# Optimization experiments

Hardware: AMD Instinct MI355X
Metric: run time of the kernel (lower is better)

The kernel has to match this reference:

```python
import jax, jax.numpy as jnp
import numpy as np

D = 768  # hidden dim hard-coded in the module


def setup_inputs() -> dict:
    key = jax.random.key(0)
    k1, k2, k3, k4, k5 = jax.random.split(key, 5)
    N, M = 512, 512
    return {
        "text_output": jax.random.normal(k1, (N, D), dtype=jnp.float32),
        "visual_output": jax.random.normal(k2, (M, D), dtype=jnp.float32),
        "W1": jax.random.normal(k3, (D, D), dtype=jnp.float32),
        "W2": jax.random.normal(k4, (D, D), dtype=jnp.float32),
        "W3": jax.random.normal(k5, (D, D), dtype=jnp.float32),
    }


def reference(text_output, visual_output, W1, W2, W3):
    # C[n,m] = tanh( (text @ W1) . visual[m] )
    C = jnp.tanh((text_output @ W1) @ visual_output.T)            # (N, M)
    W2_text = text_output @ W2                                    # (N, D)
    W3_visual = visual_output @ W3.T                              # (M, D)
    # M[n,m,:] = tanh(W2_text[n] + W3_visual[m] * C[n,m])
    Mt = jnp.tanh(W2_text[:, None, :] + W3_visual[None, :, :] * C[..., None])  # (N, M, D)
    # score[n,m] = text[n] . M[n,m]  (replaces the per-row Python loop)
    score = jnp.einsum("nd,nmd->nm", text_output, Mt)             # (N, M)
    return score
```

## Files before the change

kernel.cpp:

```cpp
#include <hip/hip_runtime.h>

#define DD   768
#define NN   512
#define MM   512

#define PRE_K 2.88539008177792681472f

typedef _Float16 h8 __attribute__((ext_vector_type(8)));
typedef __attribute__((ext_vector_type(4))) float f32x4;

__device__ __forceinline__ float fexp(float x) { return __builtin_amdgcn_exp2f(x); }
__device__ __forceinline__ float frcp(float x) { return __builtin_amdgcn_rcpf(x); }
__device__ __forceinline__ float fast_tanh(float x) {
  return 1.0f - 2.0f * frcp(fexp(PRE_K * x) + 1.0f);
}

__device__ __forceinline__ void splitf(float x, ushort& h, ushort& l) {
  const _Float16 hh = (_Float16)x;
  const _Float16 ll = (_Float16)(x - (float)hh);
  h = __builtin_bit_cast(unsigned short, hh);
  l = __builtin_bit_cast(unsigned short, ll);
}

__global__ __launch_bounds__(256) void prep_kernel(
    const float* __restrict__ text, const float* __restrict__ visual,
    const float* __restrict__ W1, const float* __restrict__ W2,
    const float* __restrict__ W3,
    ushort* __restrict__ th, ushort* __restrict__ tl,
    ushort* __restrict__ vh, ushort* __restrict__ vl,
    ushort* __restrict__ w3h, ushort* __restrict__ w3l,
    ushort* __restrict__ w1th, ushort* __restrict__ w1tl,
    ushort* __restrict__ w2th, ushort* __restrict__ w2tl)
{
  __shared__ float Lt[32][33];
  const int b = blockIdx.x;
  const int t = threadIdx.x;

  if (b < 1344) {
    const float* src; ushort *dh, *dl; size_t off;
    if (b < 384)      { src = text;   dh = th;  dl = tl;  off = (size_t)b * 1024; }
    else if (b < 768) { src = visual; dh = vh;  dl = vl;  off = (size_t)(b - 384) * 1024; }
    else              { src = W3;     dh = w3h; dl = w3l; off = (size_t)(b - 768) * 1024; }
    const size_t i = off + (size_t)t * 4;
    const float4 v = *(const float4*)&src[i];
    ushort4 h, l;
    splitf(v.x, h.x, l.x); splitf(v.y, h.y, l.y);
    splitf(v.z, h.z, l.z); splitf(v.w, h.w, l.w);
    *(ushort4*)&dh[i] = h;
    *(ushort4*)&dl[i] = l;
  } else {
    const int tt = b - 1344;
    const bool second = tt >= 576;
    const int tile = second ? tt - 576 : tt;
    const float* W = second ? W2 : W1;
    ushort* oh = second ? w2th : w1th;
    ushort* ol = second ? w2tl : w1tl;
    const int k0 = (tile / 24) * 32, j0 = (tile % 24) * 32;
    {
      const int k = t >> 3, j4 = (t & 7) * 4;
      const float4 v = *(const float4*)&W[(size_t)(k0 + k) * DD + j0 + j4];
      Lt[j4 + 0][k] = v.x; Lt[j4 + 1][k] = v.y;
      Lt[j4 + 2][k] = v.z; Lt[j4 + 3][k] = v.w;
    }
    __syncthreads();
    {
      const int j = t >> 3, k4 = (t & 7) * 4;
      ushort4 h, l;
      splitf(Lt[j][k4 + 0], h.x, l.x); splitf(Lt[j][k4 + 1], h.y, l.y);
      splitf(Lt[j][k4 + 2], h.z, l.z); splitf(Lt[j][k4 + 3], h.w, l.w);
      *(ushort4*)&oh[(size_t)(j0 + j) * DD + k0 + k4] = h;
      *(ushort4*)&ol[(size_t)(j0 + j) * DD + k0 + k4] = l;
    }
  }
}

#define BK   32
#define LROW 40

__device__ __forceinline__ void gemm_core(
    const ushort* __restrict__ Ahg, const ushort* __restrict__ Alg,
    const ushort* __restrict__ Bhg, const ushort* __restrict__ Blg,
    int i0, int j0, int k0, int nsteps, f32x4* acc)
{
  __shared__ ushort As[2][2][64 * LROW];
  __shared__ ushort Bs[2][2][64 * LROW];

  const int tid  = threadIdx.x;
  const int row  = tid >> 2;
  const int ks8  = (tid & 3) * 8;
  const size_t ga = (size_t)(i0 + row) * DD + k0 + ks8;
  const size_t gb = (size_t)(j0 + row) * DD + k0 + ks8;
  const int ldsw = row * LROW + ks8;

  const int lane = tid & 63, wave = tid >> 6;
  const int r15 = lane & 15, quad = lane >> 4;
  const int fa = (wave * 16 + r15) * LROW + quad * 8;
  const int fb = r15 * LROW + quad * 8;

  h8 pah = *(const h8*)(Ahg + ga);
  h8 pal = *(const h8*)(Alg + ga);
  h8 pbh = *(const h8*)(Bhg + gb);
  h8 pbl = *(const h8*)(Blg + gb);

  int p = 0;
  *(h8*)&As[0][0][ldsw] = pah; *(h8*)&As[0][1][ldsw] = pal;
  *(h8*)&Bs[0][0][ldsw] = pbh; *(h8*)&Bs[0][1][ldsw] = pbl;
  __syncthreads();

  for (int s = 0; s < nsteps; ++s) {
    const bool more = (s + 1 < nsteps);
    if (more) {
      pah = *(const h8*)(Ahg + ga + (s + 1) * BK);
      pal = *(const h8*)(Alg + ga + (s + 1) * BK);
      pbh = *(const h8*)(Bhg + gb + (s + 1) * BK);
      pbl = *(const h8*)(Blg + gb + (s + 1) * BK);
    }
    const h8 a_h = *(const h8*)&As[p][0][fa];
    const h8 a_l = *(const h8*)&As[p][1][fa];
    h8 b_h[4], b_l[4];
    #pragma unroll
    for (int c = 0; c < 4; ++c) {
      b_h[c] = *(const h8*)&Bs[p][0][fb + c * 16 * LROW];
      b_l[c] = *(const h8*)&Bs[p][1][fb + c * 16 * LROW];
    }
    #pragma unroll
    for (int c = 0; c < 4; ++c)
      acc[c] = __builtin_amdgcn_mfma_f32_16x16x32_f16(a_h, b_h[c], acc[c], 0, 0, 0);
    #pragma unroll
    for (int c = 0; c < 4; ++c)
      acc[c] = __builtin_amdgcn_mfma_f32_16x16x32_f16(a_h, b_l[c], acc[c], 0, 0, 0);
    #pragma unroll
    for (int c = 0; c < 4; ++c)
      acc[c] = __builtin_amdgcn_mfma_f32_16x16x32_f16(a_l, b_h[c], acc[c], 0, 0, 0);
    if (more) {
      const int q = p ^ 1;
      *(h8*)&As[q][0][ldsw] = pah; *(h8*)&As[q][1][ldsw] = pal;
      *(h8*)&Bs[q][0][ldsw] = pbh; *(h8*)&Bs[q][1][ldsw] = pbl;
    }
    __syncthreads();
    p ^= 1;
  }
}

__global__ __launch_bounds__(256) void mfma1_kernel(
    const ushort* __restrict__ th, const ushort* __restrict__ tl,
    const ushort* __restrict__ vh, const ushort* __restrict__ vl,
    const ushort* __restrict__ w1th, const ushort* __restrict__ w1tl,
    const ushort* __restrict__ w2th, const ushort* __restrict__ w2tl,
    const ushort* __restrict__ w3h, const ushort* __restrict__ w3l,
    ushort* __restrict__ Ah, ushort* __restrict__ Al,
    float* __restrict__ kw2t, float* __restrict__ kw3v)
{
  const int z  = blockIdx.z;
  const int j0 = blockIdx.x * 64;
  const int i0 = blockIdx.y * 64;
  const ushort *Arh, *Arl, *Brh, *Brl;
  if (z == 0)      { Arh = th; Arl = tl; Brh = w1th; Brl = w1tl; }
  else if (z == 1) { Arh = th; Arl = tl; Brh = w2th; Brl = w2tl; }
  else             { Arh = vh; Arl = vl; Brh = w3h;  Brl = w3l;  }

  f32x4 acc[4];
  #pragma unroll
  for (int c = 0; c < 4; ++c) acc[c] = (f32x4){0.f, 0.f, 0.f, 0.f};
  gemm_core(Arh, Arl, Brh, Brl, i0, j0, 0, DD / BK, acc);

  const int lane = threadIdx.x & 63, wave = threadIdx.x >> 6;
  const int r15 = lane & 15, quad = lane >> 4;
  if (z == 0) {
    #pragma unroll
    for (int c = 0; c < 4; ++c)
      #pragma unroll
      for (int r = 0; r < 4; ++r) {
        const size_t o = (size_t)(i0 + wave * 16 + quad * 4 + r) * DD + j0 + c * 16 + r15;
        splitf(acc[c][r], Ah[o], Al[o]);
      }
  } else {
    float* Out = (z == 1) ? kw2t : kw3v;
    #pragma unroll
    for (int c = 0; c < 4; ++c)
      #pragma unroll
      for (int r = 0; r < 4; ++r)
        Out[(size_t)(i0 + wave * 16 + quad * 4 + r) * DD + j0 + c * 16 + r15] =
            acc[c][r] * PRE_K;
  }
}

__global__ __launch_bounds__(256) void mfma2_kernel(
    const ushort* __restrict__ Ah, const ushort* __restrict__ Al,
    const ushort* __restrict__ vh, const ushort* __restrict__ vl,
    float* __restrict__ Q)
{
  const int z  = blockIdx.z;
  const int j0 = blockIdx.x * 64;
  const int i0 = blockIdx.y * 64;

  f32x4 acc[4];
  #pragma unroll
  for (int c = 0; c < 4; ++c) acc[c] = (f32x4){0.f, 0.f, 0.f, 0.f};
  gemm_core(Ah, Al, vh, vl, i0, j0, z * (DD / 4), (DD / 4) / BK, acc);

  const int lane = threadIdx.x & 63, wave = threadIdx.x >> 6;
  const int r15 = lane & 15, quad = lane >> 4;
  float* Out = Q + (size_t)z * NN * MM;
  #pragma unroll
  for (int c = 0; c < 4; ++c)
    #pragma unroll
    for (int r = 0; r < 4; ++r)
      Out[(size_t)(i0 + wave * 16 + quad * 4 + r) * MM + j0 + c * 16 + r15] = acc[c][r];
}

#define DCH    64
#define DRANGE 256
#define MLDW   68

__global__ __launch_bounds__(256) void main_kernel(
    const float* __restrict__ text, const float* __restrict__ kw2t,
    const float* __restrict__ kw3v, const float* __restrict__ Q,
    float* __restrict__ Spart)
{
  __shared__ float ts[16][MLDW];
  __shared__ float w2s[16][MLDW];
  __shared__ float w3s[32][MLDW];

  const int tid = threadIdx.x;
  const int nl = tid >> 4;
  const int ml = tid & 15;
  const int n0 = blockIdx.y * 16;
  const int m0 = blockIdx.x * 32;
  const int z  = blockIdx.z;
  const int n  = n0 + nl;
  const int mA = m0 + ml, mB = mA + 16;
  const int dbase = z * DRANGE;

  float cA = 0.f, cB = 0.f;
  #pragma unroll
  for (int zz = 0; zz < 4; ++zz) {
    const float* q = Q + (size_t)zz * NN * MM + (size_t)n * MM;
    cA += q[mA]; cB += q[mB];
  }
  cA = fast_tanh(cA); cB = fast_tanh(cB);

  float4 aA = {0.f, 0.f, 0.f, 0.f};
  float4 aB = {0.f, 0.f, 0.f, 0.f};

  const int srow = tid >> 4;
  const int sc4  = (tid & 15) << 2;

  for (int dc = 0; dc < DRANGE; dc += DCH) {
    const int d0 = dbase + dc;
    *(float4*)&ts[srow][sc4]       = *(const float4*)&text[(size_t)(n0 + srow) * DD + d0 + sc4];
    *(float4*)&w2s[srow][sc4]      = *(const float4*)&kw2t[(size_t)(n0 + srow) * DD + d0 + sc4];
    *(float4*)&w3s[srow][sc4]      = *(const float4*)&kw3v[(size_t)(m0 + srow) * DD + d0 + sc4];
    *(float4*)&w3s[srow + 16][sc4] = *(const float4*)&kw3v[(size_t)(m0 + 16 + srow) * DD + d0 + sc4];
    __syncthreads();

    #pragma unroll 4
    for (int j = 0; j < DCH; j += 4) {
      const float4 tv  = *(const float4*)&ts[nl][j];
      const float4 w2  = *(const float4*)&w2s[nl][j];
      const float4 w3A = *(const float4*)&w3s[ml][j];
      const float4 w3B = *(const float4*)&w3s[ml + 16][j];
      aA.x = fmaf(tv.x, frcp(fexp(fmaf(w3A.x, cA, w2.x)) + 1.0f), aA.x);
      aA.y = fmaf(tv.y, frcp(fexp(fmaf(w3A.y, cA, w2.y)) + 1.0f), aA.y);
      aA.z = fmaf(tv.z, frcp(fexp(fmaf(w3A.z, cA, w2.z)) + 1.0f), aA.z);
      aA.w = fmaf(tv.w, frcp(fexp(fmaf(w3A.w, cA, w2.w)) + 1.0f), aA.w);
      aB.x = fmaf(tv.x, frcp(fexp(fmaf(w3B.x, cB, w2.x)) + 1.0f), aB.x);
      aB.y = fmaf(tv.y, frcp(fexp(fmaf(w3B.y, cB, w2.y)) + 1.0f), aB.y);
      aB.z = fmaf(tv.z, frcp(fexp(fmaf(w3B.z, cB, w2.z)) + 1.0f), aB.z);
      aB.w = fmaf(tv.w, frcp(fexp(fmaf(w3B.w, cB, w2.w)) + 1.0f), aB.w);
    }
    __syncthreads();
  }

  float* Sp = Spart + (size_t)z * NN * MM + (size_t)n * MM;
  Sp[mA] = (aA.x + aA.y) + (aA.z + aA.w);
  Sp[mB] = (aB.x + aB.y) + (aB.z + aB.w);
}

__global__ __launch_bounds__(256) void combine_kernel(
    const float* __restrict__ Spart, const float* __restrict__ text,
    float* __restrict__ out)
{
  __shared__ float red[256];
  __shared__ float Tsh[2];
  const int b = blockIdx.x, t = threadIdx.x;
  const int n0 = b * 2;
  const int half = t >> 7;
  const int lt = t & 127;

  const float* tr = text + (size_t)(n0 + half) * DD;
  float s = 0.f;
  #pragma unroll
  for (int i = 0; i < DD / 128; ++i) s += tr[lt + i * 128];
  red[t] = s;
  __syncthreads();
  #pragma unroll
  for (int st = 64; st > 0; st >>= 1) {
    if (lt < st) red[t] += red[t + st];
    __syncthreads();
  }
  if (lt == 0) Tsh[half] = red[t];
  __syncthreads();

  const size_t i = (size_t)b * 1024 + (size_t)t * 4;
  const size_t S = (size_t)NN * MM;
  const float Tn = Tsh[half];
  const float4 s0 = *(const float4*)&Spart[i];
  const float4 s1 = *(const float4*)&Spart[S + i];
  const float4 s2 = *(const float4*)&Spart[2 * S + i];
  float4 o;
  o.x = Tn - 2.0f * (s0.x + s1.x + s2.x);
  o.y = Tn - 2.0f * (s0.y + s1.y + s2.y);
  o.z = Tn - 2.0f * (s0.z + s1.z + s2.z);
  o.w = Tn - 2.0f * (s0.w + s1.w + s2.w);
  *(float4*)&out[i] = o;
}

extern "C" void kernel_launch(void* const* d_in, const int* in_sizes, int n_in,
                              void* d_out, int out_size, void* d_ws, size_t ws_size,
                              hipStream_t stream) {
  const float* text   = (const float*)d_in[0];
  const float* visual = (const float*)d_in[1];
  const float* W1     = (const float*)d_in[2];
  const float* W2     = (const float*)d_in[3];
  const float* W3     = (const float*)d_in[4];
  float* out = (float*)d_out;

  char* base = (char*)d_ws;
  ushort* th   = (ushort*)(base);
  ushort* tl   = (ushort*)(base + 786432);
  ushort* vh   = (ushort*)(base + 1572864);
  ushort* vl   = (ushort*)(base + 2359296);
  ushort* w1th = (ushort*)(base + 3145728);
  ushort* w1tl = (ushort*)(base + 4325376);
  ushort* w2th = (ushort*)(base + 5505024);
  ushort* w2tl = (ushort*)(base + 6684672);
  ushort* w3h  = (ushort*)(base + 7864320);
  ushort* w3l  = (ushort*)(base + 9043968);
  ushort* Ah   = (ushort*)(base + 10223616);
  ushort* Al   = (ushort*)(base + 11010048);
  float*  kw2t = (float*) (base + 11796480);
  float*  kw3v = (float*) (base + 13369344);
  float*  Q     = (float*)(base + 3145728);
  float*  Spart = (float*)(base + 7864320);

  hipLaunchKernelGGL(prep_kernel, dim3(2496), dim3(256), 0, stream,
                     text, visual, W1, W2, W3,
                     th, tl, vh, vl, w3h, w3l, w1th, w1tl, w2th, w2tl);
  hipLaunchKernelGGL(mfma1_kernel, dim3(DD / 64, NN / 64, 3), dim3(256), 0, stream,
                     th, tl, vh, vl, w1th, w1tl, w2th, w2tl, w3h, w3l,
                     Ah, Al, kw2t, kw3v);
  hipLaunchKernelGGL(mfma2_kernel, dim3(MM / 64, NN / 64, 4), dim3(256), 0, stream,
                     Ah, Al, vh, vl, Q);
  hipLaunchKernelGGL(main_kernel, dim3(MM / 32, NN / 16, 3), dim3(256), 0, stream,
                     text, kw2t, kw3v, Q, Spart);
  hipLaunchKernelGGL(combine_kernel, dim3(NN * MM / 1024), dim3(256), 0, stream,
                     Spart, text, out);
}
```

Baseline: 140.5 us.

## Double-buffer main kernel smem loads and drop A-low MFMA pass for W2/W3 GEMMs

The main tanh-reduction kernel gets register-prefetched, double-buffered shared memory, so global loads for the next D chunk overlap the transcendental compute and one barrier per chunk is removed. The GEMM core is templated to skip the low-half correction term of the A operand for the W2·text and W3·visual products. That saves a third of the MFMAs and the A-low loads in those two GEMMs. The cost is lower precision on those projections, which feed straight into the tanh argument.

```diff
diff --git a/kernel.cpp b/kernel.cpp
--- a/kernel.cpp
+++ b/kernel.cpp
@@ -77,6 +77,7 @@
 #define BK   32
 #define LROW 40
 
+template <bool ALO>
 __device__ __forceinline__ void gemm_core(
     const ushort* __restrict__ Ahg, const ushort* __restrict__ Alg,
     const ushort* __restrict__ Bhg, const ushort* __restrict__ Blg,
@@ -98,12 +99,13 @@
   const int fb = r15 * LROW + quad * 8;
 
   h8 pah = *(const h8*)(Ahg + ga);
-  h8 pal = *(const h8*)(Alg + ga);
+  h8 pal; if (ALO) pal = *(const h8*)(Alg + ga);
   h8 pbh = *(const h8*)(Bhg + gb);
   h8 pbl = *(const h8*)(Blg + gb);
 
   int p = 0;
-  *(h8*)&As[0][0][ldsw] = pah; *(h8*)&As[0][1][ldsw] = pal;
+  *(h8*)&As[0][0][ldsw] = pah;
+  if (ALO) *(h8*)&As[0][1][ldsw] = pal;
   *(h8*)&Bs[0][0][ldsw] = pbh; *(h8*)&Bs[0][1][ldsw] = pbl;
   __syncthreads();
 
@@ -111,12 +113,12 @@
     const bool more = (s + 1 < nsteps);
     if (more) {
       pah = *(const h8*)(Ahg + ga + (s + 1) * BK);
-      pal = *(const h8*)(Alg + ga + (s + 1) * BK);
+      if (ALO) pal = *(const h8*)(Alg + ga + (s + 1) * BK);
       pbh = *(const h8*)(Bhg + gb + (s + 1) * BK);
       pbl = *(const h8*)(Blg + gb + (s + 1) * BK);
     }
     const h8 a_h = *(const h8*)&As[p][0][fa];
-    const h8 a_l = *(const h8*)&As[p][1][fa];
+    h8 a_l; if (ALO) a_l = *(const h8*)&As[p][1][fa];
     h8 b_h[4], b_l[4];
     #pragma unroll
     for (int c = 0; c < 4; ++c) {
@@ -129,12 +131,15 @@
     #pragma unroll
     for (int c = 0; c < 4; ++c)
       acc[c] = __builtin_amdgcn_mfma_f32_16x16x32_f16(a_h, b_l[c], acc[c], 0, 0, 0);
-    #pragma unroll
-    for (int c = 0; c < 4; ++c)
-      acc[c] = __builtin_amdgcn_mfma_f32_16x16x32_f16(a_l, b_h[c], acc[c], 0, 0, 0);
+    if (ALO) {
+      #pragma unroll
+      for (int c = 0; c < 4; ++c)
+        acc[c] = __builtin_amdgcn_mfma_f32_16x16x32_f16(a_l, b_h[c], acc[c], 0, 0, 0);
+    }
     if (more) {
       const int q = p ^ 1;
-      *(h8*)&As[q][0][ldsw] = pah; *(h8*)&As[q][1][ldsw] = pal;
+      *(h8*)&As[q][0][ldsw] = pah;
+      if (ALO) *(h8*)&As[q][1][ldsw] = pal;
       *(h8*)&Bs[q][0][ldsw] = pbh; *(h8*)&Bs[q][1][ldsw] = pbl;
     }
     __syncthreads();
@@ -154,15 +159,17 @@
   const int z  = blockIdx.z;
   const int j0 = blockIdx.x * 64;
   const int i0 = blockIdx.y * 64;
-  const ushort *Arh, *Arl, *Brh, *Brl;
-  if (z == 0)      { Arh = th; Arl = tl; Brh = w1th; Brl = w1tl; }
-  else if (z == 1) { Arh = th; Arl = tl; Brh = w2th; Brl = w2tl; }
-  else             { Arh = vh; Arl = vl; Brh = w3h;  Brl = w3l;  }
 
   f32x4 acc[4];
   #pragma unroll
   for (int c = 0; c < 4; ++c) acc[c] = (f32x4){0.f, 0.f, 0.f, 0.f};
-  gemm_core(Arh, Arl, Brh, Brl, i0, j0, 0, DD / BK, acc);
+
+  if (z == 0)
+    gemm_core<true >(th, tl, w1th, w1tl, i0, j0, 0, DD / BK, acc);
+  else if (z == 1)
+    gemm_core<false>(th, tl, w2th, w2tl, i0, j0, 0, DD / BK, acc);
+  else
+    gemm_core<false>(vh, vl, w3h,  w3l,  i0, j0, 0, DD / BK, acc);
 
   const int lane = threadIdx.x & 63, wave = threadIdx.x >> 6;
   const int r15 = lane & 15, quad = lane >> 4;
@@ -197,7 +204,7 @@
   f32x4 acc[4];
   #pragma unroll
   for (int c = 0; c < 4; ++c) acc[c] = (f32x4){0.f, 0.f, 0.f, 0.f};
-  gemm_core(Ah, Al, vh, vl, i0, j0, z * (DD / 4), (DD / 4) / BK, acc);
+  gemm_core<true>(Ah, Al, vh, vl, i0, j0, z * (DD / 4), (DD / 4) / BK, acc);
 
   const int lane = threadIdx.x & 63, wave = threadIdx.x >> 6;
   const int r15 = lane & 15, quad = lane >> 4;
@@ -218,9 +225,7 @@
     const float* __restrict__ kw3v, const float* __restrict__ Q,
     float* __restrict__ Spart)
 {
-  __shared__ float ts[16][MLDW];
-  __shared__ float w2s[16][MLDW];
-  __shared__ float w3s[32][MLDW];
+  __shared__ float sbuf[2][64 * MLDW];
 
   const int tid = threadIdx.x;
   const int nl = tid >> 4;
@@ -245,31 +250,60 @@
 
   const int srow = tid >> 4;
   const int sc4  = (tid & 15) << 2;
-
-  for (int dc = 0; dc < DRANGE; dc += DCH) {
-    const int d0 = dbase + dc;
-    *(float4*)&ts[srow][sc4]       = *(const float4*)&text[(size_t)(n0 + srow) * DD + d0 + sc4];
-    *(float4*)&w2s[srow][sc4]      = *(const float4*)&kw2t[(size_t)(n0 + srow) * DD + d0 + sc4];
-    *(float4*)&w3s[srow][sc4]      = *(const float4*)&kw3v[(size_t)(m0 + srow) * DD + d0 + sc4];
-    *(float4*)&w3s[srow + 16][sc4] = *(const float4*)&kw3v[(size_t)(m0 + 16 + srow) * DD + d0 + sc4];
-    __syncthreads();
-
+  const float* gt  = &text[(size_t)(n0 + srow) * DD + dbase + sc4];
+  const float* g2  = &kw2t[(size_t)(n0 + srow) * DD + dbase + sc4];
+  const float* g3a = &kw3v[(size_t)(m0 + srow) * DD + dbase + sc4];
+  const float* g3b = &kw3v[(size_t)(m0 + 16 + srow) * DD + dbase + sc4];
+  const int wt  = srow * MLDW + sc4;
+  const int w2  = (16 + srow) * MLDW + sc4;
+  const int w3a = (32 + srow) * MLDW + sc4;
+  const int w3b = (48 + srow) * MLDW + sc4;
+
+  float4 rt  = *(const float4*)gt;
+  float4 r2  = *(const float4*)g2;
+  float4 r3a = *(const float4*)g3a;
+  float4 r3b = *(const float4*)g3b;
+  int p = 0;
+  *(float4*)&sbuf[0][wt]  = rt;
+  *(float4*)&sbuf[0][w2]  = r2;
+  *(float4*)&sbuf[0][w3a] = r3a;
+  *(float4*)&sbuf[0][w3b] = r3b;
+  __syncthreads();
+
+  #pragma unroll
+  for (int c = 0; c < DRANGE / DCH; ++c) {
+    const bool more = (c + 1 < DRANGE / DCH);
+    if (more) {
+      rt  = *(const float4*)(gt  + (c + 1) * DCH);
+      r2  = *(const float4*)(g2  + (c + 1) * DCH);
+      r3a = *(const float4*)(g3a + (c + 1) * DCH);
+      r3b = *(const float4*)(g3b + (c + 1) * DCH);
+    }
+    const float* bp = sbuf[p];
     #pragma unroll 4
     for (int j = 0; j < DCH; j += 4) {
-      const float4 tv  = *(const float4*)&ts[nl][j];
-      const float4 w2  = *(const float4*)&w2s[nl][j];
-      const float4 w3A = *(const float4*)&w3s[ml][j];
-      const float4 w3B = *(const float4*)&w3s[ml + 16][j];
-      aA.x = fmaf(tv.x, frcp(fexp(fmaf(w3A.x, cA, w2.x)) + 1.0f), aA.x);
-      aA.y = fmaf(tv.y, frcp(fexp(fmaf(w3A.y, cA, w2.y)) + 1.0f), aA.y);
-      aA.z = fmaf(tv.z, frcp(fexp(fmaf(w3A.z, cA, w2.z)) + 1.0f), aA.z);
-      aA.w = fmaf(tv.w, frcp(fexp(fmaf(w3A.w, cA, w2.w)) + 1.0f), aA.w);
-      aB.x = fmaf(tv.x, frcp(fexp(fmaf(w3B.x, cB, w2.x)) + 1.0f), aB.x);
-      aB.y = fmaf(tv.y, frcp(fexp(fmaf(w3B.y, cB, w2.y)) + 1.0f), aB.y);
-      aB.z = fmaf(tv.z, frcp(fexp(fmaf(w3B.z, cB, w2.z)) + 1.0f), aB.z);
-      aB.w = fmaf(tv.w, frcp(fexp(fmaf(w3B.w, cB, w2.w)) + 1.0f), aB.w);
+      const float4 tv  = *(const float4*)&bp[nl * MLDW + j];
+      const float4 w2v = *(const float4*)&bp[(16 + nl) * MLDW + j];
+      const float4 w3A = *(const float4*)&bp[(32 + ml) * MLDW + j];
+      const float4 w3B = *(const float4*)&bp[(48 + ml) * MLDW + j];
+      aA.x = fmaf(tv.x, frcp(fexp(fmaf(w3A.x, cA, w2v.x)) + 1.0f), aA.x);
+      aA.y = fmaf(tv.y, frcp(fexp(fmaf(w3A.y, cA, w2v.y)) + 1.0f), aA.y);
+      aA.z = fmaf(tv.z, frcp(fexp(fmaf(w3A.z, cA, w2v.z)) + 1.0f), aA.z);
+      aA.w = fmaf(tv.w, frcp(fexp(fmaf(w3A.w, cA, w2v.w)) + 1.0f), aA.w);
+      aB.x = fmaf(tv.x, frcp(fexp(fmaf(w3B.x, cB, w2v.x)) + 1.0f), aB.x);
+      aB.y = fmaf(tv.y, frcp(fexp(fmaf(w3B.y, cB, w2v.y)) + 1.0f), aB.y);
+      aB.z = fmaf(tv.z, frcp(fexp(fmaf(w3B.z, cB, w2v.z)) + 1.0f), aB.z);
+      aB.w = fmaf(tv.w, frcp(fexp(fmaf(w3B.w, cB, w2v.w)) + 1.0f), aB.w);
+    }
+    if (more) {
+      const int q = p ^ 1;
+      *(float4*)&sbuf[q][wt]  = rt;
+      *(float4*)&sbuf[q][w2]  = r2;
+      *(float4*)&sbuf[q][w3a] = r3a;
+      *(float4*)&sbuf[q][w3b] = r3b;
     }
     __syncthreads();
+    p ^= 1;
   }
 
   float* Sp = Spart + (size_t)z * NN * MM + (size_t)n * MM;
```

Measured after the change: 137.8 us. About the same (-1.9%).
